# Optimization experiments

Measured on AMD Instinct MI355X. Metric: run time of the kernel, lower is better.

## Reference

```python
import jax, jax.numpy as jnp
import numpy as np

EPS = 1e-5


def _conv3x3(x, w, b):
    # x: [B,Cin,H,W], w: [Cout,Cin,3,3]
    y = jax.lax.conv_general_dilated(x, w, (1, 1), 'SAME',
                                     dimension_numbers=('NCHW', 'OIHW', 'NCHW'))
    return y + b[None, :, None, None]


def _gn_per_channel(x, w, b):
    # GroupNorm with num_groups == num_channels: per-channel spatial normalization
    mu = x.mean(axis=(2, 3), keepdims=True)
    var = x.var(axis=(2, 3), keepdims=True)
    return (x - mu) * jax.lax.rsqrt(var + EPS) * w[None, :, None, None] + b[None, :, None, None]


def _p1x1(x, w, b):
    # 1x1 conv as channel matmul. w: [Cout,Cin]
    return jnp.einsum('oc,bchw->bohw', w, x) + b[None, :, None, None]


def _cell(x, h, c, m, lc, conv_w, conv_b, gn1_w, gn1_b, convL_w, convL_b, gn2_w, gn2_b,
          wq, bq, wk, bk, wk2, bk2, wv, bv, wv2, bv2, wz, bz, wm, bm):
    # --- first conv-gate block ---
    cc = _gn_per_channel(_conv3x3(jnp.concatenate([x, h], axis=1), conv_w, conv_b), gn1_w, gn1_b)
    ci, cf, co, cg = jnp.split(cc, 4, axis=1)
    c_next = jax.nn.sigmoid(cf) * c + jax.nn.sigmoid(ci) * jnp.tanh(cg)
    # --- second (long) conv-gate block ---
    ccl = _gn_per_channel(_conv3x3(jnp.concatenate([h, c_next], axis=1), convL_w, convL_b), gn2_w, gn2_b)
    li, lf, lo, lg = jnp.split(ccl, 4, axis=1)
    lc_next = jax.nn.sigmoid(lf) * lc + jax.nn.sigmoid(li) * jnp.tanh(lg)
    c_next = jax.nn.sigmoid(lo) * jnp.tanh(lc_next)
    h_mid = jax.nn.sigmoid(co) * jnp.tanh(c_next)
    # --- SAM spatial self-attention memory ---
    B, C, H, W = h_mid.shape
    HW = H * W
    Kh = _p1x1(h_mid, wk, bk).reshape(B, -1, HW)          # [B,A,HW]
    Qh = _p1x1(h_mid, wq, bq).reshape(B, -1, HW).transpose(0, 2, 1)  # [B,HW,A]
    Vh = _p1x1(h_mid, wv, bv).reshape(B, C, HW)           # [B,C,HW]
    Km = _p1x1(m, wk2, bk2).reshape(B, -1, HW)
    Vm = _p1x1(m, wv2, bv2).reshape(B, C, HW)
    Ah = jax.nn.softmax(jnp.einsum('bpa,baq->bpq', Qh, Kh), axis=-1)  # [B,HW,HW]
    Zh = jnp.einsum('bpq,bcq->bcp', Ah, Vh).reshape(B, C, H, W)
    Am = jax.nn.softmax(jnp.einsum('bpa,baq->bpq', Qh, Km), axis=-1)
    Zm = jnp.einsum('bpq,bcq->bcp', Am, Vm).reshape(B, C, H, W)
    Z = _p1x1(jnp.concatenate([Zh, Zm], axis=1), wz, bz)  # [B,2C,H,W]
    comb = _p1x1(jnp.concatenate([Z, h_mid], axis=1), wm, bm)  # [B,3C,H,W]
    mo, mg, mi = jnp.split(comb, 3, axis=1)
    mi = jax.nn.sigmoid(mi)
    m_next = (1.0 - mi) * m + mi * jnp.tanh(mg)
    h_next = jax.nn.sigmoid(mo) * m_next
    return h_next, c_next, m_next, lc_next


def setup_inputs() -> dict:
    key = jax.random.key(0)
    B, Cin, Ch, A, H, W = 16, 64, 64, 32, 32, 32
    ks = jax.random.split(key, 24)
    s = 0.05
    inp = {
        'x': jax.random.normal(ks[0], (B, Cin, H, W), jnp.float32),
        'h': jax.random.normal(ks[1], (B, Ch, H, W), jnp.float32),
        'c': jax.random.normal(ks[2], (B, Ch, H, W), jnp.float32),
        'm': jax.random.normal(ks[3], (B, Ch, H, W), jnp.float32),
        'lc': jax.random.normal(ks[4], (B, Ch, H, W), jnp.float32),
        'conv_w': jax.random.normal(ks[5], (4 * Ch, Cin + Ch, 3, 3), jnp.float32) * s,
        'conv_b': jnp.zeros((4 * Ch,), jnp.float32),
        'gn1_w': jnp.ones((4 * Ch,), jnp.float32),
        'gn1_b': jnp.zeros((4 * Ch,), jnp.float32),
        'convL_w': jax.random.normal(ks[6], (4 * Ch, 2 * Ch, 3, 3), jnp.float32) * s,
        'convL_b': jnp.zeros((4 * Ch,), jnp.float32),
        'gn2_w': jnp.ones((4 * Ch,), jnp.float32),
        'gn2_b': jnp.zeros((4 * Ch,), jnp.float32),
        'wq': jax.random.normal(ks[7], (A, Ch), jnp.float32) * s,
        'bq': jnp.zeros((A,), jnp.float32),
        'wk': jax.random.normal(ks[8], (A, Ch), jnp.float32) * s,
        'bk': jnp.zeros((A,), jnp.float32),
        'wk2': jax.random.normal(ks[9], (A, Ch), jnp.float32) * s,
        'bk2': jnp.zeros((A,), jnp.float32),
        'wv': jax.random.normal(ks[10], (Ch, Ch), jnp.float32) * s,
        'bv': jnp.zeros((Ch,), jnp.float32),
        'wv2': jax.random.normal(ks[11], (Ch, Ch), jnp.float32) * s,
        'bv2': jnp.zeros((Ch,), jnp.float32),
        'wz': jax.random.normal(ks[12], (2 * Ch, 2 * Ch), jnp.float32) * s,
        'bz': jnp.zeros((2 * Ch,), jnp.float32),
        'wm': jax.random.normal(ks[13], (3 * Ch, 3 * Ch), jnp.float32) * s,
        'bm': jnp.zeros((3 * Ch,), jnp.float32),
    }
    return inp


def reference(x, h, c, m, lc, conv_w, conv_b, gn1_w, gn1_b, convL_w, convL_b, gn2_w, gn2_b,
              wq, bq, wk, bk, wk2, bk2, wv, bv, wv2, bv2, wz, bz, wm, bm):
    return _cell(x, h, c, m, lc, conv_w, conv_b, gn1_w, gn1_b, convL_w, convL_b, gn2_w, gn2_b,
                 wq, bq, wk, bk, wk2, bk2, wv, bv, wv2, bv2, wz, bz, wm, bm)
```

## Files before the change

kernel.cpp:

```cpp
#include <hip/hip_runtime.h>

#define DEV __device__ __forceinline__

typedef __attribute__((ext_vector_type(8))) __bf16 bf16x8;
typedef __attribute__((ext_vector_type(4))) float f32x4;
typedef __attribute__((ext_vector_type(8))) unsigned short ushort8;
typedef __attribute__((ext_vector_type(2))) unsigned short ushort2v;
typedef __attribute__((ext_vector_type(2))) unsigned int uint2v;

DEV float sigmoidf_(float x){ return 1.0f/(1.0f + __expf(-x)); }
DEV float tanhf_(float x){
    x = fminf(15.0f, fmaxf(-15.0f, x));
    float e = __expf(2.0f*x);
    return (e - 1.0f)/(e + 1.0f);
}
DEV unsigned short f2bf(float f){
    unsigned u = __builtin_bit_cast(unsigned, f);
    unsigned r = (u + 0x7FFFu + ((u>>16)&1u)) >> 16;
    return (unsigned short)r;
}
DEV float bf2f(unsigned short u){
    return __builtin_bit_cast(float, ((unsigned)u)<<16);
}
DEV unsigned cvt_pk_bf16(float lo, float hi){
    unsigned r;
    asm("v_cvt_pk_bf16_f32 %0, %1, %2" : "=v"(r) : "v"(lo), "v"(hi));
    return r;
}

__global__ __launch_bounds__(256)
void prep_kernel(const float* __restrict__ conv_w, const float* __restrict__ convL_w,
                 const float* __restrict__ wz, const float* __restrict__ wm,
                 const float* __restrict__ wq, const float* __restrict__ wk,
                 const float* __restrict__ wv, const float* __restrict__ wk2,
                 const float* __restrict__ wv2,
                 const float* __restrict__ x, const float* __restrict__ h,
                 unsigned short* __restrict__ wpk1, unsigned short* __restrict__ wpk2,
                 unsigned short* __restrict__ wzb, unsigned short* __restrict__ wmb,
                 unsigned short* __restrict__ wph, unsigned short* __restrict__ wpm,
                 unsigned short* __restrict__ buf1, unsigned short* __restrict__ buf2)
{
    __shared__ float tile[128][65];
    if (blockIdx.x < 1152) {
        int idx = blockIdx.x*256 + threadIdx.x;
        {
            int co  = idx / (128*9);
            int rem = idx - co*(128*9);
            int ci  = rem / 9;
            int tap = rem - ci*9;
            int kchunk = (ci>>5)*9 + tap;
            int o = (kchunk*256 + co)*32 + (ci&31);
            wpk1[o] = f2bf(conv_w[idx]);
            wpk2[o] = f2bf(convL_w[idx]);
        }
        if (idx < 128*128) wzb[idx] = f2bf(wz[idx]);
        if (idx < 192*192) wmb[idx] = f2bf(wm[idx]);
        if (idx < 32*64){
            wph[idx]        = f2bf(wq[idx]);
            wph[2048 + idx] = f2bf(wk[idx]);
            wpm[idx]        = f2bf(wk2[idx]);
        }
        if (idx < 64*64){
            wph[4096 + idx] = f2bf(wv[idx]);
            wpm[2048 + idx] = f2bf(wv2[idx]);
        }
    } else {
        int bx = blockIdx.x - 1152;
        int b  = bx >> 4;
        int p0 = (bx & 15) * 64;
        int t  = threadIdx.x;
        for (int k=t;k<8192;k+=256){
            int ci = k>>6, pp = k&63;
            const float* s = (ci<64) ? x + (size_t)(b*64+ci)*1024
                                     : h + (size_t)(b*64+ci-64)*1024;
            tile[ci][pp] = s[p0+pp];
        }
        __syncthreads();
        for (int k=t;k<4096;k+=256){
            int pp = k>>6, c2 = k&63;
            ushort2v v;
            v.x = f2bf(tile[c2*2][pp]);
            v.y = f2bf(tile[c2*2+1][pp]);
            *reinterpret_cast<ushort2v*>(buf1 + (size_t)(b*1024+p0+pp)*128 + c2*2) = v;
            if (c2 >= 32)
                *reinterpret_cast<ushort2v*>(buf2 + (size_t)(b*1024+p0+pp)*128 + (c2-32)*2) = v;
        }
    }
}

__global__ __launch_bounds__(256)
void conv_mfma_kernel(const unsigned short* __restrict__ inp,
                      const unsigned short* __restrict__ wpk,
                      const float* __restrict__ bias,
                      unsigned short* __restrict__ out,
                      float* __restrict__ stats)
{
    const int b   = blockIdx.z;
    const int co0 = blockIdx.y * 64;
    const int r0  = blockIdx.x * 4;
    const int t   = threadIdx.x;
    const int l   = t & 63;
    const int wv  = t >> 6;
    const int l15 = l & 15;
    const int lhi = l >> 4;

    __shared__ __align__(16) unsigned short in_t[26112];
    __shared__ float red_s[4][64];
    __shared__ float red_q[4][64];

    for (int it = t; it < 3264; it += 256) {
        int pixlin = it >> 4, oct = it & 15;
        int rr = pixlin / 34;
        int cc = pixlin - rr*34;
        int gr = r0 + rr - 1, gc = cc - 1;
        ushort8 v = {};
        if ((unsigned)gr < 32u && (unsigned)gc < 32u)
            v = *reinterpret_cast<const ushort8*>(
                    inp + ((size_t)(b*1024 + gr*32 + gc)*128) + oct*8);
        unsigned byte = (unsigned)(pixlin*256 + oct*16) ^ (((unsigned)pixlin & 7u) << 4);
        *reinterpret_cast<ushort8*>(reinterpret_cast<char*>(in_t) + byte) = v;
    }

    f32x4 acc[4][2];
#pragma unroll
    for (int i=0;i<4;i++)
#pragma unroll
        for (int f=0;f<2;f++)
            acc[i][f] = (f32x4){0.f,0.f,0.f,0.f};

    __syncthreads();

    bf16x8 afc[4], bfc[2], afn[4], bfn[2];
#define LDA_(K, DST) do { const unsigned short* wrow_ = wpk + ((K)*256 + co0)*32; \
        for (int i_=0;i_<4;i_++) DST[i_] = *reinterpret_cast<const bf16x8*>(wrow_ + (i_*16 + l15)*32 + lhi*8); } while(0)
#define LDB_(K, DST) do { const int cic_ = (K)/9, tap_ = (K) - 9*((K)/9); \
        const int ky_ = tap_/3, kx_ = tap_ - 3*(tap_/3); \
        for (int f_=0;f_<2;f_++){ int pixlin_ = (wv + ky_)*34 + (f_*16 + l15 + kx_); \
            unsigned byte_ = (unsigned)(pixlin_*256 + cic_*64 + lhi*16) ^ (((unsigned)pixlin_ & 7u) << 4); \
            DST[f_] = *reinterpret_cast<const bf16x8*>(reinterpret_cast<const char*>(in_t) + byte_); } } while(0)

    LDA_(0, afc); LDB_(0, bfc);
#pragma unroll
    for (int k=0; k<36; ++k){
        if (k < 35){ LDA_(k+1, afn); LDB_(k+1, bfn); }
#pragma unroll
        for (int i=0;i<4;i++){
            acc[i][0] = __builtin_amdgcn_mfma_f32_16x16x32_bf16(afc[i], bfc[0], acc[i][0], 0,0,0);
            acc[i][1] = __builtin_amdgcn_mfma_f32_16x16x32_bf16(afc[i], bfc[1], acc[i][1], 0,0,0);
        }
        if (k < 35){
#pragma unroll
            for (int i=0;i<4;i++) afc[i] = afn[i];
            bfc[0] = bfn[0]; bfc[1] = bfn[1];
        }
    }
#undef LDA_
#undef LDB_

    const int orow = r0 + wv;
    float s_ir[4][4], q_ir[4][4];
#pragma unroll
    for (int i=0;i<4;i++){
        int cobase = co0 + i*16 + lhi*4;
#pragma unroll
        for (int r=0;r<4;r++){
            float bs = bias[cobase+r];
            float e0 = acc[i][0][r] + bs;
            float e1 = acc[i][1][r] + bs;
            out[(size_t)(b*256 + cobase + r)*1024 + orow*32 + l15]      = f2bf(e0);
            out[(size_t)(b*256 + cobase + r)*1024 + orow*32 + 16 + l15] = f2bf(e1);
            s_ir[i][r] = e0 + e1;
            q_ir[i][r] = e0*e0 + e1*e1;
        }
    }
#pragma unroll
    for (int i=0;i<4;i++)
#pragma unroll
        for (int r=0;r<4;r++){
            float s = s_ir[i][r], q = q_ir[i][r];
            s += __shfl_xor(s,1); q += __shfl_xor(q,1);
            s += __shfl_xor(s,2); q += __shfl_xor(q,2);
            s += __shfl_xor(s,4); q += __shfl_xor(q,4);
            s += __shfl_xor(s,8); q += __shfl_xor(q,8);
            s_ir[i][r] = s; q_ir[i][r] = q;
        }
    if (l15 == 0){
#pragma unroll
        for (int i=0;i<4;i++)
#pragma unroll
            for (int r=0;r<4;r++){
                red_s[wv][i*16 + lhi*4 + r] = s_ir[i][r];
                red_q[wv][i*16 + lhi*4 + r] = q_ir[i][r];
            }
    }
    __syncthreads();
    if (t < 64){
        float S = red_s[0][t]+red_s[1][t]+red_s[2][t]+red_s[3][t];
        float Q = red_q[0][t]+red_q[1][t]+red_q[2][t]+red_q[3][t];
        float* sp = stats + ((size_t)(b*256 + co0 + t)*8 + blockIdx.x)*2;
        sp[0] = S; sp[1] = Q;
    }
}

__global__ __launch_bounds__(256)
void gn_gate1_kernel(const unsigned short* __restrict__ cc, const float* __restrict__ stats,
                     const float* __restrict__ gnw, const float* __restrict__ gnb,
                     const float* __restrict__ c_in,
                     unsigned short* __restrict__ buf2, unsigned short* __restrict__ sig_pm)
{
    const int b  = blockIdx.y;
    const int p0 = blockIdx.x * 64;
    const int t  = threadIdx.x;
    __shared__ float sc[256][2];
    __shared__ __align__(16) unsigned short cct[16384];

    {
        const float* sp = stats + (size_t)(b*256 + t)*16;
        float S=0.f, Q=0.f;
#pragma unroll
        for (int k=0;k<8;k++){ S += sp[2*k]; Q += sp[2*k+1]; }
        float mu  = S*(1.0f/1024.0f);
        float var = Q*(1.0f/1024.0f) - mu*mu;
        float rs  = rsqrtf(var + 1e-5f);
        float gw  = gnw[t];
        sc[t][0] = rs*gw;
        sc[t][1] = gnb[t] - mu*rs*gw;
    }
    for (int it=t; it<2048; it+=256){
        int row = it>>3, oct = it&7;
        ushort8 v = *reinterpret_cast<const ushort8*>(
            cc + (size_t)(b*256+row)*1024 + p0 + oct*8);
        unsigned byte = (unsigned)(row*128) + (((unsigned)oct*16) ^ ((unsigned)(row&7)<<4));
        *reinterpret_cast<ushort8*>(reinterpret_cast<char*>(cct) + byte) = v;
    }
    __syncthreads();

    const int p = t & 63, cg = t >> 6;
    float cn[16], so[16];
#pragma unroll
    for (int j=0;j<16;j++){
        int ch = cg*16 + j;
        float xg[4];
#pragma unroll
        for (int g=0; g<4; g++){
            int row = g*64 + ch;
            unsigned byte = (unsigned)(row*128) + (((unsigned)(p*2)) ^ ((unsigned)(row&7)<<4));
            float v = bf2f(*reinterpret_cast<const unsigned short*>(
                reinterpret_cast<const char*>(cct) + byte));
            xg[g] = v*sc[row][0] + sc[row][1];
        }
        float cv = c_in[(size_t)(b*64+ch)*1024 + p0 + p];
        cn[j] = sigmoidf_(xg[1])*cv + sigmoidf_(xg[0])*tanhf_(xg[3]);
        so[j] = sigmoidf_(xg[2]);
    }
    ushort8 v0, v1, s0, s1;
#pragma unroll
    for (int j=0;j<8;j++){
        v0[j]=f2bf(cn[j]); v1[j]=f2bf(cn[8+j]);
        s0[j]=f2bf(so[j]); s1[j]=f2bf(so[8+j]);
    }
    size_t prow = (size_t)(b*1024 + p0 + p);
    *reinterpret_cast<ushort8*>(buf2 + prow*128 + 64 + cg*16)     = v0;
    *reinterpret_cast<ushort8*>(buf2 + prow*128 + 64 + cg*16 + 8) = v1;
    *reinterpret_cast<ushort8*>(sig_pm + prow*64 + cg*16)     = s0;
    *reinterpret_cast<ushort8*>(sig_pm + prow*64 + cg*16 + 8) = s1;
}

__global__ __launch_bounds__(256)
void gn2_proj_kernel(const unsigned short* __restrict__ cc, const float* __restrict__ stats,
                     const float* __restrict__ gnw, const float* __restrict__ gnb,
                     const float* __restrict__ lc_in, const unsigned short* __restrict__ sig_pm,
                     const float* __restrict__ m_in,
                     const unsigned short* __restrict__ wph, const unsigned short* __restrict__ wpm,
                     const float* __restrict__ bq, const float* __restrict__ bk,
                     const float* __restrict__ bv, const float* __restrict__ bk2,
                     const float* __restrict__ bv2,
                     float* __restrict__ out_lc, float* __restrict__ out_c,
                     unsigned short* __restrict__ hT,
                     unsigned short* __restrict__ Qb, unsigned short* __restrict__ Khb,
                     unsigned short* __restrict__ Kmb,
                     unsigned short* __restrict__ Vhb, unsigned short* __restrict__ Vmb)
{
    const int b  = blockIdx.y;
    const int p0 = blockIdx.x * 64;
    const int t  = threadIdx.x;
    const int l  = t & 63;
    const int w  = t >> 6;
    const int l15 = l & 15, lhi = l >> 4;

    __shared__ float sc[256][2];
    __shared__ __align__(16) unsigned short cct[16384];

    {
        const float* sp = stats + (size_t)(b*256 + t)*16;
        float S=0.f, Q=0.f;
#pragma unroll
        for (int k=0;k<8;k++){ S += sp[2*k]; Q += sp[2*k+1]; }
        float mu  = S*(1.0f/1024.0f);
        float var = Q*(1.0f/1024.0f) - mu*mu;
        float rs  = rsqrtf(var + 1e-5f);
        float gw  = gnw[t];
        sc[t][0] = rs*gw;
        sc[t][1] = gnb[t] - mu*rs*gw;
    }
    for (int it=t; it<2048; it+=256){
        int row = it>>3, oct = it&7;
        ushort8 v = *reinterpret_cast<const ushort8*>(
            cc + (size_t)(b*256+row)*1024 + p0 + oct*8);
        unsigned byte = (unsigned)(row*128) + (((unsigned)oct*16) ^ ((unsigned)(row&7)<<4));
        *reinterpret_cast<ushort8*>(reinterpret_cast<char*>(cct) + byte) = v;
    }
    __syncthreads();

    const int p = t & 63, cg = t >> 6;
    const size_t prow = (size_t)(b*1024 + p0 + p);
    float hm[16], mr[16];
    {
        ushort8 sv0 = *reinterpret_cast<const ushort8*>(sig_pm + prow*64 + cg*16);
        ushort8 sv1 = *reinterpret_cast<const ushort8*>(sig_pm + prow*64 + cg*16 + 8);
        float sof[16];
#pragma unroll
        for (int j=0;j<8;j++){ sof[j] = bf2f(sv0[j]); sof[8+j] = bf2f(sv1[j]); }
#pragma unroll
        for (int j=0;j<16;j++){
            int ch = cg*16 + j;
            float xg[4];
#pragma unroll
            for (int g=0; g<4; g++){
                int row = g*64 + ch;
                unsigned byte = (unsigned)(row*128) + (((unsigned)(p*2)) ^ ((unsigned)(row&7)<<4));
                float v = bf2f(*reinterpret_cast<const unsigned short*>(
                    reinterpret_cast<const char*>(cct) + byte));
                xg[g] = v*sc[row][0] + sc[row][1];
            }
            float lv  = lc_in[(size_t)(b*64+ch)*1024 + p0 + p];
            float lcn = sigmoidf_(xg[1])*lv + sigmoidf_(xg[0])*tanhf_(xg[3]);
            float cnx = sigmoidf_(xg[2])*tanhf_(lcn);
            out_lc[(size_t)(b*64+ch)*1024 + p0 + p] = lcn;
            out_c [(size_t)(b*64+ch)*1024 + p0 + p] = cnx;
            hm[j] = sof[j]*tanhf_(cnx);
            mr[j] = m_in[(size_t)(b*64+ch)*1024 + p0 + p];
        }
    }
    __syncthreads();

    {
        ushort8 h0,h1,m0,m1;
#pragma unroll
        for (int j=0;j<8;j++){
            h0[j]=f2bf(hm[j]); h1[j]=f2bf(hm[8+j]);
            m0[j]=f2bf(mr[j]); m1[j]=f2bf(mr[8+j]);
        }
        unsigned hb0 = (unsigned)(p*128) + (((unsigned)(cg*32))    ^ ((unsigned)(p&7)<<4));
        unsigned hb1 = (unsigned)(p*128) + (((unsigned)(cg*32+16)) ^ ((unsigned)(p&7)<<4));
        *reinterpret_cast<ushort8*>(reinterpret_cast<char*>(cct) + hb0) = h0;
        *reinterpret_cast<ushort8*>(reinterpret_cast<char*>(cct) + hb1) = h1;
        *reinterpret_cast<ushort8*>(reinterpret_cast<char*>(cct) + 8192 + hb0) = m0;
        *reinterpret_cast<ushort8*>(reinterpret_cast<char*>(cct) + 8192 + hb1) = m1;
        *reinterpret_cast<ushort8*>(hT + prow*64 + cg*16)     = h0;
        *reinterpret_cast<ushort8*>(hT + prow*64 + cg*16 + 8) = h1;
    }
    __syncthreads();

    const int pix = w*16 + l15;
    const unsigned xsw = ((unsigned)(pix&7)) << 4;
    f32x4 dh[8], dm[6];
#pragma unroll
    for (int i=0;i<8;i++) dh[i] = (f32x4){0.f,0.f,0.f,0.f};
#pragma unroll
    for (int i=0;i<6;i++) dm[i] = (f32x4){0.f,0.f,0.f,0.f};
#pragma unroll
    for (int ks=0; ks<2; ++ks){
        unsigned xb = (unsigned)(pix*128) + (((unsigned)(ks*64 + lhi*16)) ^ xsw);
        bf16x8 xh = *reinterpret_cast<const bf16x8*>(reinterpret_cast<const char*>(cct) + xb);
        bf16x8 xm = *reinterpret_cast<const bf16x8*>(reinterpret_cast<const char*>(cct) + 8192 + xb);
#pragma unroll
        for (int ocf=0; ocf<8; ocf++){
            bf16x8 af = *reinterpret_cast<const bf16x8*>(
                wph + (size_t)(ocf*16 + l15)*64 + ks*32 + lhi*8);
            dh[ocf] = __builtin_amdgcn_mfma_f32_16x16x32_bf16(af, xh, dh[ocf], 0,0,0);
        }
#pragma unroll
        for (int ocf=0; ocf<6; ocf++){
            bf16x8 am = *reinterpret_cast<const bf16x8*>(
                wpm + (size_t)(ocf*16 + l15)*64 + ks*32 + lhi*8);
            dm[ocf] = __builtin_amdgcn_mfma_f32_16x16x32_bf16(am, xm, dm[ocf], 0,0,0);
        }
    }
#pragma unroll
    for (int ocf=0; ocf<4; ocf++)
#pragma unroll
        for (int r=0;r<4;r++){
            int vc = ocf*16 + lhi*4 + r;
            Vhb[(size_t)(b*64+vc)*1024 + p0 + pix] = f2bf(dh[4+ocf][r] + bv[vc]);
            Vmb[(size_t)(b*64+vc)*1024 + p0 + pix] = f2bf(dm[2+ocf][r] + bv2[vc]);
        }
#pragma unroll
    for (int ocf=0; ocf<2; ocf++)
#pragma unroll
        for (int r=0;r<4;r++){
            int qc = ocf*16 + lhi*4 + r;
            unsigned byq = (unsigned)(pix*128) + (((unsigned)(qc*2))      ^ xsw);
            unsigned byk = (unsigned)(pix*128) + (((unsigned)(64 + qc*2)) ^ xsw);
            *reinterpret_cast<unsigned short*>(reinterpret_cast<char*>(cct) + 16384 + byq)
                = f2bf(dh[ocf][r]   + bq[qc]);
            *reinterpret_cast<unsigned short*>(reinterpret_cast<char*>(cct) + 16384 + byk)
                = f2bf(dh[2+ocf][r] + bk[qc]);
        }
    __syncthreads();
    for (int it=t; it<512; it+=256){
        int pr = it>>3, oct = it&7;
        unsigned byte = (unsigned)(pr*128) + (((unsigned)(oct*16)) ^ ((unsigned)(pr&7)<<4));
        ushort8 v = *reinterpret_cast<const ushort8*>(
            reinterpret_cast<const char*>(cct) + 16384 + byte);
        if (oct < 4) *reinterpret_cast<ushort8*>(Qb  + (size_t)(b*1024+p0+pr)*32 + oct*8) = v;
        else         *reinterpret_cast<ushort8*>(Khb + (size_t)(b*1024+p0+pr)*32 + (oct-4)*8) = v;
    }
    __syncthreads();
#pragma unroll
    for (int ocf=0; ocf<2; ocf++)
#pragma unroll
        for (int r=0;r<4;r++){
            int qc = ocf*16 + lhi*4 + r;
            unsigned byq = (unsigned)(pix*128) + (((unsigned)(qc*2)) ^ xsw);
            *reinterpret_cast<unsigned short*>(reinterpret_cast<char*>(cct) + 16384 + byq)
                = f2bf(dm[ocf][r] + bk2[qc]);
        }
    __syncthreads();
    {
        int pr = t>>2, oct = t&3;
        unsigned byte = (unsigned)(pr*128) + (((unsigned)(oct*16)) ^ ((unsigned)(pr&7)<<4));
        ushort8 v = *reinterpret_cast<const ushort8*>(
            reinterpret_cast<const char*>(cct) + 16384 + byte);
        *reinterpret_cast<ushort8*>(Kmb + (size_t)(b*1024+p0+pr)*32 + oct*8) = v;
    }
}

__global__ __launch_bounds__(256)
void attn_final_kernel(const unsigned short* __restrict__ Qb,
                       const unsigned short* __restrict__ Kh,
                       const unsigned short* __restrict__ Km,
                       const unsigned short* __restrict__ Vh,
                       const unsigned short* __restrict__ Vm,
                       const unsigned short* __restrict__ hT,
                       const unsigned short* __restrict__ wzb,
                       const unsigned short* __restrict__ wmb,
                       const float* __restrict__ bz, const float* __restrict__ bm,
                       const float* __restrict__ m_in,
                       float* __restrict__ out_h, float* __restrict__ out_m)
{
    const int bid  = blockIdx.x;
    const int xcd  = bid & 7;
    const int slot = bid >> 3;
    const int b    = xcd*2 + (slot>>5);
    const int p0   = (slot & 31) * 32;
    const int t   = threadIdx.x;
    const int l   = t & 63;
    const int w   = t >> 6;
    const int l15 = l & 15, g = l >> 4;
    const int pass = w >> 1;
    const int ph   = w & 1;

    __shared__ __align__(16) unsigned short Kt[2][2][2560];
    __shared__ __align__(16) unsigned short Vt[2][2][4096];
    __shared__ __align__(16) unsigned short Pt[2][2048];
    __shared__ __align__(16) unsigned short Bs[32*192];

    const bf16x8 qa = *reinterpret_cast<const bf16x8*>(
        Qb + (size_t)(b*1024 + p0 + ph*16 + l15)*32 + g*8);

    float m_run = -1e30f, l_run = 0.0f;
    f32x4 acc[4];
#pragma unroll
    for (int cf=0;cf<4;cf++) acc[cf] = (f32x4){0.f,0.f,0.f,0.f};

    const int krow = t>>2, koct = t&3;
    const int vrow = t>>3, voct = t&7;
    const unsigned kwb  = (unsigned)(krow*80 + koct*16);
    const unsigned vwb0 = (unsigned)(vrow*128)      + (((unsigned)voct*16) ^ ((unsigned)(vrow&7)<<4));
    const unsigned vwb1 = (unsigned)((vrow+32)*128) + (((unsigned)voct*16) ^ ((unsigned)((vrow+32)&7)<<4));

    ushort8 kr0, kr1, vv0, vv1, vv2, vv3;
#define LDSTAGE(Q0N) do { \
        kr0 = *reinterpret_cast<const ushort8*>(Kh + (size_t)(b*1024 + (Q0N) + krow)*32 + koct*8); \
        kr1 = *reinterpret_cast<const ushort8*>(Km + (size_t)(b*1024 + (Q0N) + krow)*32 + koct*8); \
        vv0 = *reinterpret_cast<const ushort8*>(Vh + (size_t)(b*64 + vrow)*1024 + (Q0N) + voct*8); \
        vv1 = *reinterpret_cast<const ushort8*>(Vh + (size_t)(b*64 + vrow+32)*1024 + (Q0N) + voct*8); \
        vv2 = *reinterpret_cast<const ushort8*>(Vm + (size_t)(b*64 + vrow)*1024 + (Q0N) + voct*8); \
        vv3 = *reinterpret_cast<const ushort8*>(Vm + (size_t)(b*64 + vrow+32)*1024 + (Q0N) + voct*8); \
    } while(0)
#define WRSTAGE(BUF) do { \
        *reinterpret_cast<ushort8*>(reinterpret_cast<char*>(Kt[0][BUF]) + kwb)  = kr0; \
        *reinterpret_cast<ushort8*>(reinterpret_cast<char*>(Kt[1][BUF]) + kwb)  = kr1; \
        *reinterpret_cast<ushort8*>(reinterpret_cast<char*>(Vt[0][BUF]) + vwb0) = vv0; \
        *reinterpret_cast<ushort8*>(reinterpret_cast<char*>(Vt[0][BUF]) + vwb1) = vv1; \
        *reinterpret_cast<ushort8*>(reinterpret_cast<char*>(Vt[1][BUF]) + vwb0) = vv2; \
        *reinterpret_cast<ushort8*>(reinterpret_cast<char*>(Vt[1][BUF]) + vwb1) = vv3; \
    } while(0)

    LDSTAGE(0);
    WRSTAGE(0);
    __syncthreads();

    const unsigned prow = (unsigned)(ph*16 + l15);
    const unsigned psw  = (prow & 7u) << 4;
    char* Pbase = reinterpret_cast<char*>(Pt[pass]);

    for (int it=0; it<16; ++it){
        const int cur = it & 1;
        if (it < 15) LDSTAGE((it+1)*64);

        f32x4 s2[4];
#pragma unroll
        for (int qt=0; qt<4; qt++){
            const bf16x8 kb = *reinterpret_cast<const bf16x8*>(
                reinterpret_cast<const char*>(Kt[pass][cur]) + (qt*16 + l15)*80 + g*16);
            s2[qt] = __builtin_amdgcn_mfma_f32_16x16x32_bf16(kb, qa, (f32x4){0.f,0.f,0.f,0.f}, 0,0,0);
        }

        float pm = s2[0][0];
#pragma unroll
        for (int qt=0; qt<4; qt++)
#pragma unroll
            for (int r=0;r<4;r++) pm = fmaxf(pm, s2[qt][r]);
        pm = fmaxf(pm, __shfl_xor(pm, 16));
        pm = fmaxf(pm, __shfl_xor(pm, 32));

        if (!__all(pm <= m_run + 8.0f)){
            float mn = fmaxf(m_run, pm);
            float f  = __expf(m_run - mn);
            m_run = mn;
            l_run *= f;
#pragma unroll
            for (int r=0;r<4;r++){
                float fr = __shfl(f, (l & 48) | ((l>>4)*4 + r), 64);
#pragma unroll
                for (int cf=0;cf<4;cf++) acc[cf][r] *= fr;
            }
        }

        float e[4][4];
        float lsum = 0.f;
#pragma unroll
        for (int qt=0; qt<4; qt++)
#pragma unroll
            for (int r=0;r<4;r++){
                float ev = __expf(s2[qt][r] - m_run);
                e[qt][r] = ev;
                lsum += ev;
            }
        lsum += __shfl_xor(lsum, 16);
        lsum += __shfl_xor(lsum, 32);
        l_run += lsum;

#pragma unroll
        for (int qt=0; qt<4; qt++){
            uint2v pk;
            pk.x = cvt_pk_bf16(e[qt][0], e[qt][1]);
            pk.y = cvt_pk_bf16(e[qt][2], e[qt][3]);
            unsigned byte = prow*128 + (((unsigned)(qt*32 + g*8)) ^ psw);
            *reinterpret_cast<uint2v*>(Pbase + byte) = pk;
        }

#pragma unroll
        for (int ks=0;ks<2;ks++){
            unsigned abyte = prow*128 + (((unsigned)(ks*64 + g*16)) ^ psw);
            const bf16x8 pa = *reinterpret_cast<const bf16x8*>(Pbase + abyte);
#pragma unroll
            for (int cf=0;cf<4;cf++){
                unsigned vrw = (unsigned)(cf*16 + l15);
                unsigned vbyte = vrw*128 + (((unsigned)(ks*64 + g*16)) ^ ((vrw&7u)<<4));
                const bf16x8 vb = *reinterpret_cast<const bf16x8*>(
                    reinterpret_cast<const char*>(Vt[pass][cur]) + vbyte);
                acc[cf] = __builtin_amdgcn_mfma_f32_16x16x32_bf16(pa, vb, acc[cf], 0,0,0);
            }
        }

        if (it < 15) WRSTAGE(cur^1);
        __syncthreads();
    }
#undef LDSTAGE
#undef WRSTAGE

    {
        float rl = 1.0f / l_run;
        float rr[4];
#pragma unroll
        for (int r=0;r<4;r++) rr[r] = __shfl(rl, (l & 48) | ((l>>4)*4 + r), 64);
#pragma unroll
        for (int cf=0;cf<4;cf++)
#pragma unroll
            for (int r=0;r<4;r++){
                unsigned pix = (unsigned)(ph*16 + g*4 + r);
                unsigned cch = (unsigned)(pass*64 + cf*16 + l15);
                unsigned byte = pix*384 + ((cch*2) ^ ((pix&7u)<<4));
                *reinterpret_cast<unsigned short*>(reinterpret_cast<char*>(Bs) + byte)
                    = f2bf(acc[cf][r]*rr[r]);
            }
    }
    {
        int row = t>>3, oct = t&7;
        ushort8 v = *reinterpret_cast<const ushort8*>(
            hT + (size_t)(b*1024 + p0 + row)*64 + oct*8);
        unsigned byte = (unsigned)(row*384) + 256u + (((unsigned)oct*16) ^ ((unsigned)(row&7)<<4));
        *reinterpret_cast<ushort8*>(reinterpret_cast<char*>(Bs) + byte) = v;
    }
    __syncthreads();

    f32x4 acc1[2][2];
#pragma unroll
    for (int i=0;i<2;i++)
#pragma unroll
        for (int cf=0;cf<2;cf++) acc1[i][cf] = (f32x4){0.f,0.f,0.f,0.f};
#pragma unroll
    for (int ks=0; ks<4; ++ks){
        bf16x8 af[2];
#pragma unroll
        for (int i=0;i<2;i++)
            af[i] = *reinterpret_cast<const bf16x8*>(
                wzb + (size_t)(w*32 + i*16 + l15)*128 + ks*32 + g*8);
#pragma unroll
        for (int cf=0;cf<2;cf++){
            unsigned p = (unsigned)(cf*16 + l15);
            unsigned byte = p*384 + (((unsigned)(ks*64 + g*16)) ^ ((p&7u)<<4));
            const bf16x8 bfr = *reinterpret_cast<const bf16x8*>(
                reinterpret_cast<const char*>(Bs) + byte);
            acc1[0][cf] = __builtin_amdgcn_mfma_f32_16x16x32_bf16(af[0], bfr, acc1[0][cf], 0,0,0);
            acc1[1][cf] = __builtin_amdgcn_mfma_f32_16x16x32_bf16(af[1], bfr, acc1[1][cf], 0,0,0);
        }
    }
    __syncthreads();
#pragma unroll
    for (int i=0;i<2;i++){
        int co = w*32 + i*16 + g*4;
#pragma unroll
        for (int cf=0;cf<2;cf++){
            unsigned p = (unsigned)(cf*16 + l15);
#pragma unroll
            for (int r=0;r<4;r++){
                float val = acc1[i][cf][r] + bz[co+r];
                unsigned byte = p*384 + (((unsigned)((co+r)*2)) ^ ((p&7u)<<4));
                *reinterpret_cast<unsigned short*>(reinterpret_cast<char*>(Bs) + byte) = f2bf(val);
            }
        }
    }
    __syncthreads();

    f32x4 acc2[3][2];
#pragma unroll
    for (int j=0;j<3;j++)
#pragma unroll
        for (int cf=0;cf<2;cf++) acc2[j][cf] = (f32x4){0.f,0.f,0.f,0.f};
#pragma unroll
    for (int ks=0; ks<6; ++ks){
        bf16x8 am[3];
#pragma unroll
        for (int j=0;j<3;j++)
            am[j] = *reinterpret_cast<const bf16x8*>(
                wmb + (size_t)(j*64 + w*16 + l15)*192 + ks*32 + g*8);
#pragma unroll
        for (int cf=0;cf<2;cf++){
            unsigned p = (unsigned)(cf*16 + l15);
            unsigned byte = p*384 + (((unsigned)(ks*64 + g*16)) ^ ((p&7u)<<4));
            const bf16x8 bfr = *reinterpret_cast<const bf16x8*>(
                reinterpret_cast<const char*>(Bs) + byte);
#pragma unroll
            for (int j=0;j<3;j++)
                acc2[j][cf] = __builtin_amdgcn_mfma_f32_16x16x32_bf16(am[j], bfr, acc2[j][cf], 0,0,0);
        }
    }

    const int ch0 = w*16 + g*4;
#pragma unroll
    for (int cf=0;cf<2;cf++){
        int pix = p0 + cf*16 + l15;
#pragma unroll
        for (int r=0;r<4;r++){
            int ch = ch0 + r;
            float mo = acc2[0][cf][r] + bm[ch];
            float mg = acc2[1][cf][r] + bm[64+ch];
            float mi = sigmoidf_(acc2[2][cf][r] + bm[128+ch]);
            float mv = m_in[(size_t)(b*64+ch)*1024 + pix];
            float mn = (1.0f - mi)*mv + mi*tanhf_(mg);
            out_m[(size_t)(b*64+ch)*1024 + pix] = mn;
            out_h[(size_t)(b*64+ch)*1024 + pix] = sigmoidf_(mo)*mn;
        }
    }
}

extern "C" void kernel_launch(void* const* d_in, const int* in_sizes, int n_in,
                              void* d_out, int out_size, void* d_ws, size_t ws_size,
                              hipStream_t stream)
{
    const float* x      = (const float*)d_in[0];
    const float* h      = (const float*)d_in[1];
    const float* c      = (const float*)d_in[2];
    const float* m      = (const float*)d_in[3];
    const float* lc     = (const float*)d_in[4];
    const float* conv_w = (const float*)d_in[5];
    const float* conv_b = (const float*)d_in[6];
    const float* gn1_w  = (const float*)d_in[7];
    const float* gn1_b  = (const float*)d_in[8];
    const float* convL_w= (const float*)d_in[9];
    const float* convL_b= (const float*)d_in[10];
    const float* gn2_w  = (const float*)d_in[11];
    const float* gn2_b  = (const float*)d_in[12];
    const float* wq  = (const float*)d_in[13];
    const float* bq  = (const float*)d_in[14];
    const float* wk  = (const float*)d_in[15];
    const float* bk  = (const float*)d_in[16];
    const float* wk2 = (const float*)d_in[17];
    const float* bk2 = (const float*)d_in[18];
    const float* wv  = (const float*)d_in[19];
    const float* bv  = (const float*)d_in[20];
    const float* wv2 = (const float*)d_in[21];
    const float* bv2 = (const float*)d_in[22];
    const float* wz  = (const float*)d_in[23];
    const float* bz  = (const float*)d_in[24];
    const float* wmw = (const float*)d_in[25];
    const float* bm  = (const float*)d_in[26];

    float* out = (float*)d_out;
    float* F = (float*)d_ws;
    unsigned short* cc_bf  = (unsigned short*)F;
    unsigned short* buf1   = (unsigned short*)(F + 4194304);
    unsigned short* buf2   = (unsigned short*)(F + 5242880);
    unsigned short* hT     = (unsigned short*)(F + 6291456);
    unsigned short* Qb     = (unsigned short*)(F + 6815744);
    unsigned short* Khb    = (unsigned short*)(F + 7077888);
    unsigned short* Kmb    = (unsigned short*)(F + 7340032);
    unsigned short* Vhb    = (unsigned short*)(F + 7602176);
    unsigned short* Vmb    = (unsigned short*)(F + 8126464);
    unsigned short* sig_pm = (unsigned short*)(F + 8650752);
    unsigned short* wpk1   = (unsigned short*)(F + 9175040);
    unsigned short* wpk2   = (unsigned short*)(F + 9322496);
    unsigned short* wzb    = (unsigned short*)(F + 9469952);
    unsigned short* wmb    = (unsigned short*)(F + 9478144);
    unsigned short* wph    = (unsigned short*)(F + 9496576);
    unsigned short* wpm    = (unsigned short*)(F + 9500672);
    float*          stats  = F + 9503744;

    dim3 blk256(256);
    prep_kernel<<<dim3(1408), blk256, 0, stream>>>(conv_w, convL_w, wz, wmw,
                                                   wq, wk, wv, wk2, wv2, x, h,
                                                   wpk1, wpk2, wzb, wmb, wph, wpm,
                                                   buf1, buf2);
    dim3 cgrid(8, 4, 16);
    conv_mfma_kernel<<<cgrid, blk256, 0, stream>>>(buf1, wpk1, conv_b, cc_bf, stats);
    gn_gate1_kernel<<<dim3(16,16), blk256, 0, stream>>>(cc_bf, stats, gn1_w, gn1_b, c,
                                                        buf2, sig_pm);
    conv_mfma_kernel<<<cgrid, blk256, 0, stream>>>(buf2, wpk2, convL_b, cc_bf, stats);
    gn2_proj_kernel<<<dim3(16,16), blk256, 0, stream>>>(cc_bf, stats, gn2_w, gn2_b,
                                                        lc, sig_pm, m, wph, wpm,
                                                        bq, bk, bv, bk2, bv2,
                                                        out + 3*1048576 ,
                                                        out + 1*1048576 ,
                                                        hT, Qb, Khb, Kmb, Vhb, Vmb);
    attn_final_kernel<<<dim3(512), blk256, 0, stream>>>(Qb, Khb, Kmb, Vhb, Vmb, hT,
                                                        wzb, wmb, bz, bm, m,
                                                        out , out + 2*1048576 );
    (void)in_sizes; (void)n_in; (void)out_size; (void)ws_size;
}
```

Before: 127.5 us.

## Halve per-block tiles in conv, gate and projection kernels to double grid sizes

The 3x3 conv kernel now covers 2 output rows per block instead of 4, with each wave handling a 16-pixel half-row, and the launch grid doubles to 1024 blocks. GroupNorm partial stats grow from 8 to 16 slices per channel, and the gate and projection kernels are rebuilt around 32-pixel tiles with padded LDS rows instead of swizzled ones. The projection kernel now runs the h and m projections on separate wave pairs and drops the extra syncthreads rounds. The aim is more blocks and higher occupancy on the many CUs; the cost is more halo reloads, fewer MFMAs per weight load, and more stats slices to reduce.

Measured after the change: 151.0 us. 18.4% more time.

```diff
diff --git a/kernel.cpp b/kernel.cpp
--- a/kernel.cpp
+++ b/kernel.cpp
@@ -88,7 +88,7 @@
     }
 }
 
-__global__ __launch_bounds__(256)
+__global__ __launch_bounds__(256, 4)
 void conv_mfma_kernel(const unsigned short* __restrict__ inp,
                       const unsigned short* __restrict__ wpk,
                       const float* __restrict__ bias,
@@ -97,18 +97,20 @@
 {
     const int b   = blockIdx.z;
     const int co0 = blockIdx.y * 64;
-    const int r0  = blockIdx.x * 4;
+    const int r0  = blockIdx.x * 2;
     const int t   = threadIdx.x;
     const int l   = t & 63;
     const int wv  = t >> 6;
     const int l15 = l & 15;
     const int lhi = l >> 4;
-
-    __shared__ __align__(16) unsigned short in_t[26112];
+    const int wrow = wv & 1;
+    const int wcol = wv >> 1;
+
+    __shared__ __align__(16) unsigned short in_t[17408];
     __shared__ float red_s[4][64];
     __shared__ float red_q[4][64];
 
-    for (int it = t; it < 3264; it += 256) {
+    for (int it = t; it < 2176; it += 256) {
         int pixlin = it >> 4, oct = it & 15;
         int rr = pixlin / 34;
         int cc = pixlin - rr*34;
@@ -121,56 +123,49 @@
         *reinterpret_cast<ushort8*>(reinterpret_cast<char*>(in_t) + byte) = v;
     }
 
-    f32x4 acc[4][2];
-#pragma unroll
-    for (int i=0;i<4;i++)
-#pragma unroll
-        for (int f=0;f<2;f++)
-            acc[i][f] = (f32x4){0.f,0.f,0.f,0.f};
-
-    __syncthreads();
-
-    bf16x8 afc[4], bfc[2], afn[4], bfn[2];
+    f32x4 acc[4];
+#pragma unroll
+    for (int i=0;i<4;i++) acc[i] = (f32x4){0.f,0.f,0.f,0.f};
+
+    __syncthreads();
+
+    bf16x8 afc[4], afn[4];
 #define LDA_(K, DST) do { const unsigned short* wrow_ = wpk + ((K)*256 + co0)*32; \
         for (int i_=0;i_<4;i_++) DST[i_] = *reinterpret_cast<const bf16x8*>(wrow_ + (i_*16 + l15)*32 + lhi*8); } while(0)
-#define LDB_(K, DST) do { const int cic_ = (K)/9, tap_ = (K) - 9*((K)/9); \
-        const int ky_ = tap_/3, kx_ = tap_ - 3*(tap_/3); \
-        for (int f_=0;f_<2;f_++){ int pixlin_ = (wv + ky_)*34 + (f_*16 + l15 + kx_); \
-            unsigned byte_ = (unsigned)(pixlin_*256 + cic_*64 + lhi*16) ^ (((unsigned)pixlin_ & 7u) << 4); \
-            DST[f_] = *reinterpret_cast<const bf16x8*>(reinterpret_cast<const char*>(in_t) + byte_); } } while(0)
-
-    LDA_(0, afc); LDB_(0, bfc);
+
+    LDA_(0, afc);
 #pragma unroll
     for (int k=0; k<36; ++k){
-        if (k < 35){ LDA_(k+1, afn); LDB_(k+1, bfn); }
-#pragma unroll
-        for (int i=0;i<4;i++){
-            acc[i][0] = __builtin_amdgcn_mfma_f32_16x16x32_bf16(afc[i], bfc[0], acc[i][0], 0,0,0);
-            acc[i][1] = __builtin_amdgcn_mfma_f32_16x16x32_bf16(afc[i], bfc[1], acc[i][1], 0,0,0);
-        }
+        if (k < 35) LDA_(k+1, afn);
+        const int cic = k/9, tap = k - 9*(k/9);
+        const int ky = tap/3, kx = tap - 3*(tap/3);
+        int pixlin = (wrow + ky)*34 + (wcol*16 + l15 + kx);
+        unsigned byte = (unsigned)(pixlin*256 + cic*64 + lhi*16)
+                        ^ (((unsigned)pixlin & 7u) << 4);
+        bf16x8 bfr = *reinterpret_cast<const bf16x8*>(
+                         reinterpret_cast<const char*>(in_t) + byte);
+#pragma unroll
+        for (int i=0;i<4;i++)
+            acc[i] = __builtin_amdgcn_mfma_f32_16x16x32_bf16(afc[i], bfr, acc[i], 0,0,0);
         if (k < 35){
 #pragma unroll
             for (int i=0;i<4;i++) afc[i] = afn[i];
-            bfc[0] = bfn[0]; bfc[1] = bfn[1];
         }
     }
 #undef LDA_
-#undef LDB_
-
-    const int orow = r0 + wv;
+
+    const int orow = r0 + wrow;
+    const int ocol = wcol*16 + l15;
     float s_ir[4][4], q_ir[4][4];
 #pragma unroll
     for (int i=0;i<4;i++){
         int cobase = co0 + i*16 + lhi*4;
 #pragma unroll
         for (int r=0;r<4;r++){
-            float bs = bias[cobase+r];
-            float e0 = acc[i][0][r] + bs;
-            float e1 = acc[i][1][r] + bs;
-            out[(size_t)(b*256 + cobase + r)*1024 + orow*32 + l15]      = f2bf(e0);
-            out[(size_t)(b*256 + cobase + r)*1024 + orow*32 + 16 + l15] = f2bf(e1);
-            s_ir[i][r] = e0 + e1;
-            q_ir[i][r] = e0*e0 + e1*e1;
+            float e0 = acc[i][r] + bias[cobase+r];
+            out[(size_t)(b*256 + cobase + r)*1024 + orow*32 + ocol] = f2bf(e0);
+            s_ir[i][r] = e0;
+            q_ir[i][r] = e0*e0;
         }
     }
 #pragma unroll
@@ -197,7 +192,7 @@
     if (t < 64){
         float S = red_s[0][t]+red_s[1][t]+red_s[2][t]+red_s[3][t];
         float Q = red_q[0][t]+red_q[1][t]+red_q[2][t]+red_q[3][t];
-        float* sp = stats + ((size_t)(b*256 + co0 + t)*8 + blockIdx.x)*2;
+        float* sp = stats + ((size_t)(b*256 + co0 + t)*16 + blockIdx.x)*2;
         sp[0] = S; sp[1] = Q;
     }
 }
@@ -209,16 +204,16 @@
                      unsigned short* __restrict__ buf2, unsigned short* __restrict__ sig_pm)
 {
     const int b  = blockIdx.y;
-    const int p0 = blockIdx.x * 64;
+    const int p0 = blockIdx.x * 32;
     const int t  = threadIdx.x;
     __shared__ float sc[256][2];
-    __shared__ __align__(16) unsigned short cct[16384];
+    __shared__ __align__(16) unsigned short cct[10240];
 
     {
-        const float* sp = stats + (size_t)(b*256 + t)*16;
+        const float* sp = stats + (size_t)(b*256 + t)*32;
         float S=0.f, Q=0.f;
 #pragma unroll
-        for (int k=0;k<8;k++){ S += sp[2*k]; Q += sp[2*k+1]; }
+        for (int k=0;k<16;k++){ S += sp[2*k]; Q += sp[2*k+1]; }
         float mu  = S*(1.0f/1024.0f);
         float var = Q*(1.0f/1024.0f) - mu*mu;
         float rs  = rsqrtf(var + 1e-5f);
@@ -226,44 +221,36 @@
         sc[t][0] = rs*gw;
         sc[t][1] = gnb[t] - mu*rs*gw;
     }
-    for (int it=t; it<2048; it+=256){
-        int row = it>>3, oct = it&7;
+    for (int it=t; it<1024; it+=256){
+        int row = it>>2, oct = it&3;
         ushort8 v = *reinterpret_cast<const ushort8*>(
             cc + (size_t)(b*256+row)*1024 + p0 + oct*8);
-        unsigned byte = (unsigned)(row*128) + (((unsigned)oct*16) ^ ((unsigned)(row&7)<<4));
-        *reinterpret_cast<ushort8*>(reinterpret_cast<char*>(cct) + byte) = v;
-    }
-    __syncthreads();
-
-    const int p = t & 63, cg = t >> 6;
-    float cn[16], so[16];
-#pragma unroll
-    for (int j=0;j<16;j++){
-        int ch = cg*16 + j;
+        *reinterpret_cast<ushort8*>(cct + row*40 + oct*8) = v;
+    }
+    __syncthreads();
+
+    const int p = t & 31, cg = t >> 5;
+    float cn[8], so[8];
+#pragma unroll
+    for (int j=0;j<8;j++){
+        int ch = cg*8 + j;
         float xg[4];
 #pragma unroll
         for (int g=0; g<4; g++){
             int row = g*64 + ch;
-            unsigned byte = (unsigned)(row*128) + (((unsigned)(p*2)) ^ ((unsigned)(row&7)<<4));
-            float v = bf2f(*reinterpret_cast<const unsigned short*>(
-                reinterpret_cast<const char*>(cct) + byte));
+            float v = bf2f(cct[row*40 + p]);
             xg[g] = v*sc[row][0] + sc[row][1];
         }
         float cv = c_in[(size_t)(b*64+ch)*1024 + p0 + p];
         cn[j] = sigmoidf_(xg[1])*cv + sigmoidf_(xg[0])*tanhf_(xg[3]);
         so[j] = sigmoidf_(xg[2]);
     }
-    ushort8 v0, v1, s0, s1;
-#pragma unroll
-    for (int j=0;j<8;j++){
-        v0[j]=f2bf(cn[j]); v1[j]=f2bf(cn[8+j]);
-        s0[j]=f2bf(so[j]); s1[j]=f2bf(so[8+j]);
-    }
+    ushort8 v0, s0;
+#pragma unroll
+    for (int j=0;j<8;j++){ v0[j]=f2bf(cn[j]); s0[j]=f2bf(so[j]); }
     size_t prow = (size_t)(b*1024 + p0 + p);
-    *reinterpret_cast<ushort8*>(buf2 + prow*128 + 64 + cg*16)     = v0;
-    *reinterpret_cast<ushort8*>(buf2 + prow*128 + 64 + cg*16 + 8) = v1;
-    *reinterpret_cast<ushort8*>(sig_pm + prow*64 + cg*16)     = s0;
-    *reinterpret_cast<ushort8*>(sig_pm + prow*64 + cg*16 + 8) = s1;
+    *reinterpret_cast<ushort8*>(buf2 + prow*128 + 64 + cg*8) = v0;
+    *reinterpret_cast<ushort8*>(sig_pm + prow*64 + cg*8)     = s0;
 }
 
 __global__ __launch_bounds__(256)
@@ -282,20 +269,20 @@
                      unsigned short* __restrict__ Vhb, unsigned short* __restrict__ Vmb)
 {
     const int b  = blockIdx.y;
-    const int p0 = blockIdx.x * 64;
+    const int p0 = blockIdx.x * 32;
     const int t  = threadIdx.x;
     const int l  = t & 63;
     const int w  = t >> 6;
     const int l15 = l & 15, lhi = l >> 4;
 
     __shared__ float sc[256][2];
-    __shared__ __align__(16) unsigned short cct[16384];
+    __shared__ __align__(16) unsigned short cct[10240];
 
     {
-        const float* sp = stats + (size_t)(b*256 + t)*16;
+        const float* sp = stats + (size_t)(b*256 + t)*32;
         float S=0.f, Q=0.f;
 #pragma unroll
-        for (int k=0;k<8;k++){ S += sp[2*k]; Q += sp[2*k+1]; }
+        for (int k=0;k<16;k++){ S += sp[2*k]; Q += sp[2*k+1]; }
         float mu  = S*(1.0f/1024.0f);
         float var = Q*(1.0f/1024.0f) - mu*mu;
         float rs  = rsqrtf(var + 1e-5f);
@@ -303,34 +290,27 @@
         sc[t][0] = rs*gw;
         sc[t][1] = gnb[t] - mu*rs*gw;
     }
-    for (int it=t; it<2048; it+=256){
-        int row = it>>3, oct = it&7;
+    for (int it=t; it<1024; it+=256){
+        int row = it>>2, oct = it&3;
         ushort8 v = *reinterpret_cast<const ushort8*>(
             cc + (size_t)(b*256+row)*1024 + p0 + oct*8);
-        unsigned byte = (unsigned)(row*128) + (((unsigned)oct*16) ^ ((unsigned)(row&7)<<4));
-        *reinterpret_cast<ushort8*>(reinterpret_cast<char*>(cct) + byte) = v;
-    }
-    __syncthreads();
-
-    const int p = t & 63, cg = t >> 6;
+        *reinterpret_cast<ushort8*>(cct + row*40 + oct*8) = v;
+    }
+    __syncthreads();
+
+    const int p = t & 31, cg = t >> 5;
     const size_t prow = (size_t)(b*1024 + p0 + p);
-    float hm[16], mr[16];
+    float hm[8], mr[8];
     {
-        ushort8 sv0 = *reinterpret_cast<const ushort8*>(sig_pm + prow*64 + cg*16);
-        ushort8 sv1 = *reinterpret_cast<const ushort8*>(sig_pm + prow*64 + cg*16 + 8);
-        float sof[16];
-#pragma unroll
-        for (int j=0;j<8;j++){ sof[j] = bf2f(sv0[j]); sof[8+j] = bf2f(sv1[j]); }
-#pragma unroll
-        for (int j=0;j<16;j++){
-            int ch = cg*16 + j;
+        ushort8 sv = *reinterpret_cast<const ushort8*>(sig_pm + prow*64 + cg*8);
+#pragma unroll
+        for (int j=0;j<8;j++){
+            int ch = cg*8 + j;
             float xg[4];
 #pragma unroll
             for (int g=0; g<4; g++){
                 int row = g*64 + ch;
-                unsigned byte = (unsigned)(row*128) + (((unsigned)(p*2)) ^ ((unsigned)(row&7)<<4));
-                float v = bf2f(*reinterpret_cast<const unsigned short*>(
-                    reinterpret_cast<const char*>(cct) + byte));
+                float v = bf2f(cct[row*40 + p]);
                 xg[g] = v*sc[row][0] + sc[row][1];
             }
             float lv  = lc_in[(size_t)(b*64+ch)*1024 + p0 + p];
@@ -338,100 +318,108 @@
             float cnx = sigmoidf_(xg[2])*tanhf_(lcn);
             out_lc[(size_t)(b*64+ch)*1024 + p0 + p] = lcn;
             out_c [(size_t)(b*64+ch)*1024 + p0 + p] = cnx;
-            hm[j] = sof[j]*tanhf_(cnx);
+            hm[j] = bf2f(sv[j])*tanhf_(cnx);
             mr[j] = m_in[(size_t)(b*64+ch)*1024 + p0 + p];
         }
     }
     __syncthreads();
 
     {
-        ushort8 h0,h1,m0,m1;
-#pragma unroll
-        for (int j=0;j<8;j++){
-            h0[j]=f2bf(hm[j]); h1[j]=f2bf(hm[8+j]);
-            m0[j]=f2bf(mr[j]); m1[j]=f2bf(mr[8+j]);
-        }
-        unsigned hb0 = (unsigned)(p*128) + (((unsigned)(cg*32))    ^ ((unsigned)(p&7)<<4));
-        unsigned hb1 = (unsigned)(p*128) + (((unsigned)(cg*32+16)) ^ ((unsigned)(p&7)<<4));
-        *reinterpret_cast<ushort8*>(reinterpret_cast<char*>(cct) + hb0) = h0;
-        *reinterpret_cast<ushort8*>(reinterpret_cast<char*>(cct) + hb1) = h1;
-        *reinterpret_cast<ushort8*>(reinterpret_cast<char*>(cct) + 8192 + hb0) = m0;
-        *reinterpret_cast<ushort8*>(reinterpret_cast<char*>(cct) + 8192 + hb1) = m1;
-        *reinterpret_cast<ushort8*>(hT + prow*64 + cg*16)     = h0;
-        *reinterpret_cast<ushort8*>(hT + prow*64 + cg*16 + 8) = h1;
-    }
-    __syncthreads();
-
-    const int pix = w*16 + l15;
+        ushort8 h0, m0;
+#pragma unroll
+        for (int j=0;j<8;j++){ h0[j]=f2bf(hm[j]); m0[j]=f2bf(mr[j]); }
+        unsigned hb = (unsigned)(p*128) + (((unsigned)(cg*16)) ^ ((unsigned)(p&7)<<4));
+        *reinterpret_cast<ushort8*>(reinterpret_cast<char*>(cct) + hb) = h0;
+        *reinterpret_cast<ushort8*>(reinterpret_cast<char*>(cct) + 4096 + hb) = m0;
+        *reinterpret_cast<ushort8*>(hT + prow*64 + cg*8) = h0;
+    }
+    __syncthreads();
+
+    const int pass = w >> 1;
+    const int pix  = (w&1)*16 + l15;
     const unsigned xsw = ((unsigned)(pix&7)) << 4;
-    f32x4 dh[8], dm[6];
-#pragma unroll
-    for (int i=0;i<8;i++) dh[i] = (f32x4){0.f,0.f,0.f,0.f};
-#pragma unroll
-    for (int i=0;i<6;i++) dm[i] = (f32x4){0.f,0.f,0.f,0.f};
-#pragma unroll
-    for (int ks=0; ks<2; ++ks){
-        unsigned xb = (unsigned)(pix*128) + (((unsigned)(ks*64 + lhi*16)) ^ xsw);
-        bf16x8 xh = *reinterpret_cast<const bf16x8*>(reinterpret_cast<const char*>(cct) + xb);
-        bf16x8 xm = *reinterpret_cast<const bf16x8*>(reinterpret_cast<const char*>(cct) + 8192 + xb);
-#pragma unroll
-        for (int ocf=0; ocf<8; ocf++){
-            bf16x8 af = *reinterpret_cast<const bf16x8*>(
-                wph + (size_t)(ocf*16 + l15)*64 + ks*32 + lhi*8);
-            dh[ocf] = __builtin_amdgcn_mfma_f32_16x16x32_bf16(af, xh, dh[ocf], 0,0,0);
-        }
-#pragma unroll
-        for (int ocf=0; ocf<6; ocf++){
-            bf16x8 am = *reinterpret_cast<const bf16x8*>(
-                wpm + (size_t)(ocf*16 + l15)*64 + ks*32 + lhi*8);
-            dm[ocf] = __builtin_amdgcn_mfma_f32_16x16x32_bf16(am, xm, dm[ocf], 0,0,0);
-        }
-    }
-#pragma unroll
-    for (int ocf=0; ocf<4; ocf++)
-#pragma unroll
-        for (int r=0;r<4;r++){
-            int vc = ocf*16 + lhi*4 + r;
-            Vhb[(size_t)(b*64+vc)*1024 + p0 + pix] = f2bf(dh[4+ocf][r] + bv[vc]);
-            Vmb[(size_t)(b*64+vc)*1024 + p0 + pix] = f2bf(dm[2+ocf][r] + bv2[vc]);
-        }
-#pragma unroll
-    for (int ocf=0; ocf<2; ocf++)
-#pragma unroll
-        for (int r=0;r<4;r++){
-            int qc = ocf*16 + lhi*4 + r;
-            unsigned byq = (unsigned)(pix*128) + (((unsigned)(qc*2))      ^ xsw);
-            unsigned byk = (unsigned)(pix*128) + (((unsigned)(64 + qc*2)) ^ xsw);
-            *reinterpret_cast<unsigned short*>(reinterpret_cast<char*>(cct) + 16384 + byq)
-                = f2bf(dh[ocf][r]   + bq[qc]);
-            *reinterpret_cast<unsigned short*>(reinterpret_cast<char*>(cct) + 16384 + byk)
-                = f2bf(dh[2+ocf][r] + bk[qc]);
-        }
-    __syncthreads();
-    for (int it=t; it<512; it+=256){
-        int pr = it>>3, oct = it&7;
+    if (pass == 0){
+        f32x4 dh[8];
+#pragma unroll
+        for (int i=0;i<8;i++) dh[i] = (f32x4){0.f,0.f,0.f,0.f};
+#pragma unroll
+        for (int ks=0; ks<2; ++ks){
+            unsigned xb = (unsigned)(pix*128) + (((unsigned)(ks*64 + lhi*16)) ^ xsw);
+            bf16x8 xh = *reinterpret_cast<const bf16x8*>(reinterpret_cast<const char*>(cct) + xb);
+#pragma unroll
+            for (int ocf=0; ocf<8; ocf++){
+                bf16x8 af = *reinterpret_cast<const bf16x8*>(
+                    wph + (size_t)(ocf*16 + l15)*64 + ks*32 + lhi*8);
+                dh[ocf] = __builtin_amdgcn_mfma_f32_16x16x32_bf16(af, xh, dh[ocf], 0,0,0);
+            }
+        }
+#pragma unroll
+        for (int ocf=0; ocf<4; ocf++)
+#pragma unroll
+            for (int r=0;r<4;r++){
+                int vc = ocf*16 + lhi*4 + r;
+                Vhb[(size_t)(b*64+vc)*1024 + p0 + pix] = f2bf(dh[4+ocf][r] + bv[vc]);
+            }
+#pragma unroll
+        for (int ocf=0; ocf<2; ocf++)
+#pragma unroll
+            for (int r=0;r<4;r++){
+                int qc = ocf*16 + lhi*4 + r;
+                unsigned byq = (unsigned)(pix*128) + (((unsigned)(qc*2))      ^ xsw);
+                unsigned byk = (unsigned)(pix*128) + (((unsigned)(64 + qc*2)) ^ xsw);
+                *reinterpret_cast<unsigned short*>(reinterpret_cast<char*>(cct) + 8192 + byq)
+                    = f2bf(dh[ocf][r]   + bq[qc]);
+                *reinterpret_cast<unsigned short*>(reinterpret_cast<char*>(cct) + 8192 + byk)
+                    = f2bf(dh[2+ocf][r] + bk[qc]);
+            }
+    } else {
+        f32x4 dm[6];
+#pragma unroll
+        for (int i=0;i<6;i++) dm[i] = (f32x4){0.f,0.f,0.f,0.f};
+#pragma unroll
+        for (int ks=0; ks<2; ++ks){
+            unsigned xb = (unsigned)(pix*128) + (((unsigned)(ks*64 + lhi*16)) ^ xsw);
+            bf16x8 xm = *reinterpret_cast<const bf16x8*>(
+                reinterpret_cast<const char*>(cct) + 4096 + xb);
+#pragma unroll
+            for (int ocf=0; ocf<6; ocf++){
+                bf16x8 am = *reinterpret_cast<const bf16x8*>(
+                    wpm + (size_t)(ocf*16 + l15)*64 + ks*32 + lhi*8);
+                dm[ocf] = __builtin_amdgcn_mfma_f32_16x16x32_bf16(am, xm, dm[ocf], 0,0,0);
+            }
+        }
+#pragma unroll
+        for (int ocf=0; ocf<4; ocf++)
+#pragma unroll
+            for (int r=0;r<4;r++){
+                int vc = ocf*16 + lhi*4 + r;
+                Vmb[(size_t)(b*64+vc)*1024 + p0 + pix] = f2bf(dm[2+ocf][r] + bv2[vc]);
+            }
+#pragma unroll
+        for (int ocf=0; ocf<2; ocf++)
+#pragma unroll
+            for (int r=0;r<4;r++){
+                int qc = ocf*16 + lhi*4 + r;
+                unsigned byq = (unsigned)(pix*128) + (((unsigned)(qc*2)) ^ xsw);
+                *reinterpret_cast<unsigned short*>(reinterpret_cast<char*>(cct) + 12288 + byq)
+                    = f2bf(dm[ocf][r] + bk2[qc]);
+            }
+    }
+    __syncthreads();
+
+    {
+        int pr = t>>3, oct = t&7;
         unsigned byte = (unsigned)(pr*128) + (((unsigned)(oct*16)) ^ ((unsigned)(pr&7)<<4));
         ushort8 v = *reinterpret_cast<const ushort8*>(
-            reinterpret_cast<const char*>(cct) + 16384 + byte);
+            reinterpret_cast<const char*>(cct) + 8192 + byte);
         if (oct < 4) *reinterpret_cast<ushort8*>(Qb  + (size_t)(b*1024+p0+pr)*32 + oct*8) = v;
         else         *reinterpret_cast<ushort8*>(Khb + (size_t)(b*1024+p0+pr)*32 + (oct-4)*8) = v;
     }
-    __syncthreads();
-#pragma unroll
-    for (int ocf=0; ocf<2; ocf++)
-#pragma unroll
-        for (int r=0;r<4;r++){
-            int qc = ocf*16 + lhi*4 + r;
-            unsigned byq = (unsigned)(pix*128) + (((unsigned)(qc*2)) ^ xsw);
-            *reinterpret_cast<unsigned short*>(reinterpret_cast<char*>(cct) + 16384 + byq)
-                = f2bf(dm[ocf][r] + bk2[qc]);
-        }
-    __syncthreads();
-    {
+    if (t < 128){
         int pr = t>>2, oct = t&3;
         unsigned byte = (unsigned)(pr*128) + (((unsigned)(oct*16)) ^ ((unsigned)(pr&7)<<4));
         ushort8 v = *reinterpret_cast<const ushort8*>(
-            reinterpret_cast<const char*>(cct) + 16384 + byte);
+            reinterpret_cast<const char*>(cct) + 12288 + byte);
         *reinterpret_cast<ushort8*>(Kmb + (size_t)(b*1024+p0+pr)*32 + oct*8) = v;
     }
 }
@@ -745,12 +733,12 @@
                                                    wq, wk, wv, wk2, wv2, x, h,
                                                    wpk1, wpk2, wzb, wmb, wph, wpm,
                                                    buf1, buf2);
-    dim3 cgrid(8, 4, 16);
+    dim3 cgrid(16, 4, 16);
     conv_mfma_kernel<<<cgrid, blk256, 0, stream>>>(buf1, wpk1, conv_b, cc_bf, stats);
-    gn_gate1_kernel<<<dim3(16,16), blk256, 0, stream>>>(cc_bf, stats, gn1_w, gn1_b, c,
+    gn_gate1_kernel<<<dim3(32,16), blk256, 0, stream>>>(cc_bf, stats, gn1_w, gn1_b, c,
                                                         buf2, sig_pm);
     conv_mfma_kernel<<<cgrid, blk256, 0, stream>>>(buf2, wpk2, convL_b, cc_bf, stats);
-    gn2_proj_kernel<<<dim3(16,16), blk256, 0, stream>>>(cc_bf, stats, gn2_w, gn2_b,
+    gn2_proj_kernel<<<dim3(32,16), blk256, 0, stream>>>(cc_bf, stats, gn2_w, gn2_b,
                                                         lc, sig_pm, m, wph, wpm,
                                                         bq, bk, bv, bk2, bv2,
                                                         out + 3*1048576 ,
```
